# Kernel optimization log

Hardware: AMD Instinct MI355X
Metric: run time of the kernel (lower is better)

## Reference

```python
import jax, jax.numpy as jnp
import numpy as np


def _hfreq_mask(c, scale):
    # zeros over the centered (shifted) low-frequency band, ones elsewhere
    m = np.ones((c,), dtype=np.complex64)
    m[c // 2 - c // scale: c // 2 + c // scale] = 0
    return jnp.asarray(m).reshape(1, 1, 1, c)


def setup_inputs() -> dict:
    key = jax.random.key(0)
    x = jax.random.normal(key, (32, 38, 38, 728), dtype=jnp.float32)
    return {"x": x, "scale": 4}


def reference(x, scale):
    c = x.shape[-1]
    norm = jnp.asarray(np.sqrt(c), dtype=jnp.complex64)
    X = jnp.fft.fft(x.astype(jnp.complex64), axis=-1) / norm
    X = jnp.fft.fftshift(X, axes=-1)
    X = X * _hfreq_mask(c, scale)
    X = jnp.fft.ifftshift(X, axes=-1)
    y = jnp.fft.ifft(X, axis=-1) * norm
    y = jnp.real(y).astype(jnp.float32)
    return jax.nn.relu(y)
```

## Files before the change

### kernel.cpp

```cpp
#include <hip/hip_runtime.h>
#include <hip/hip_bf16.h>

#define CC 728
#define PP 364
#define KP 384
#define M_ROWS 46208
#define KT 12
#define NWG 2166

typedef __attribute__((ext_vector_type(8))) short bf16x8;
typedef __attribute__((ext_vector_type(8))) unsigned short ushort8;
typedef __attribute__((ext_vector_type(4))) float f32x4;

__device__ __forceinline__ unsigned short f2bf(float f) {
    unsigned int u = __float_as_uint(f);
    unsigned int r = u + 0x7fffu + ((u >> 16) & 1u);
    return (unsigned short)(r >> 16);
}

__device__ __forceinline__ void gload_lds16(const void* g, void* l) {
    __builtin_amdgcn_global_load_lds(
        (const __attribute__((address_space(1))) void*)g,
        (__attribute__((address_space(3))) void*)l,
        16, 0, 0);
}

__global__ void build_bt(unsigned short* __restrict__ bt1,
                         unsigned short* __restrict__ bt2) {
    int idx = blockIdx.x * blockDim.x + threadIdx.x;
    if (idx >= 2 * KP * KP) return;
    int mat = idx / (KP * KP);
    int rem = idx % (KP * KP);
    int n = rem / KP, k = rem % KP;
    float v = 0.f;
    if (n < PP && k < PP) {
        int m = n - k - (mat == 0 ? 1 : 0);
        if (m < 0) m += PP;
        int d = 2 * m + 1;
        float t = (float)(3.14159265358979323846 * (double)d / (double)CC);
        float s = ((d >> 1) & 1) ? 1.f : -1.f;
        v = s * cosf(t) / ((float)CC * sinf(t));
    }
    (mat == 0 ? bt1 : bt2)[n * KP + k] = f2bf(v);
}

__global__ __launch_bounds__(256) void gemm_relu(
        const float* __restrict__ x,
        const unsigned short* __restrict__ bt1,
        const unsigned short* __restrict__ bt2,
        float* __restrict__ out) {
    __shared__ unsigned short ldsE[64 * 32];
    __shared__ unsigned short ldsO[64 * 32];
    __shared__ unsigned short ldsB1[128 * 32];
    __shared__ unsigned short ldsB2[128 * 32];

    const int tid  = threadIdx.x;
    const int lane = tid & 63;
    const int wid  = tid >> 6;
    const int wr   = wid >> 1, wc = wid & 1;
    const int l15  = lane & 15, lhi = lane >> 4;

    const int NX = 8;
    int orig = blockIdx.x;
    int q = NWG / NX, r = NWG % NX;
    int xcd = orig % NX, local = orig / NX;
    int wgid = (xcd < r ? xcd * (q + 1) : r * (q + 1) + (xcd - r) * q) + local;
    const int bm  = (wgid / 3) * 64;
    const int bnp = (wgid % 3) * 128;

    f32x4 acc_e[2][4], acc_o[2][4];
#pragma unroll
    for (int i = 0; i < 2; ++i)
#pragma unroll
        for (int j = 0; j < 4; ++j)
#pragma unroll
            for (int rr = 0; rr < 4; ++rr) { acc_e[i][j][rr] = 0.f; acc_o[i][j][rr] = 0.f; }

    const int brow = tid >> 2;
    const int bc   = tid & 3;
    const int arow = tid >> 2;
    const int acx  = tid & 3;

    for (int kt = 0; kt < KT; ++kt) {
        const int k0 = kt * 32;

#pragma unroll
        for (int i = 0; i < 2; ++i) {
            int rr   = i * 64 + brow;
            int gsrc = (bc - (rr >> 1)) & 3;
            size_t so = (size_t)(bnp + rr) * KP + k0 + gsrc * 8;
            gload_lds16(bt1 + so, &ldsB1[(i * 256 + tid) * 8]);
            gload_lds16(bt2 + so, &ldsB2[(i * 256 + tid) * 8]);
        }

        float4 va[4];
        {
            int cb0 = 2 * k0 + acx * 16;
            const float* src = x + (size_t)(bm + arow) * CC + cb0;
#pragma unroll
            for (int i = 0; i < 4; ++i)
                va[i] = (cb0 + 4 * i < CC) ? ((const float4*)src)[i]
                                           : make_float4(0.f, 0.f, 0.f, 0.f);
        }

        {
            ushort8 oe, oo;
#pragma unroll
            for (int p = 0; p < 4; ++p) {
                float4 f = va[p];
                oe[2 * p]     = f2bf(f.x); oo[2 * p]     = f2bf(f.y);
                oe[2 * p + 1] = f2bf(f.z); oo[2 * p + 1] = f2bf(f.w);
            }
            int sc = (acx + (arow >> 1)) & 3;
            *(ushort8*)&ldsE[arow * 32 + sc * 8] = oe;
            *(ushort8*)&ldsO[arow * 32 + sc * 8] = oo;
        }
        __syncthreads();

        bf16x8 aE[2], aO[2], b1[4], b2[4];
#pragma unroll
        for (int mi = 0; mi < 2; ++mi) {
            int row = wr * 32 + mi * 16 + l15;
            int c   = (lhi + (row >> 1)) & 3;
            aE[mi] = *(const bf16x8*)&ldsE[row * 32 + c * 8];
            aO[mi] = *(const bf16x8*)&ldsO[row * 32 + c * 8];
        }
#pragma unroll
        for (int nj = 0; nj < 4; ++nj) {
            int row = wc * 64 + nj * 16 + l15;
            int c   = (lhi + (row >> 1)) & 3;
            b1[nj] = *(const bf16x8*)&ldsB1[row * 32 + c * 8];
            b2[nj] = *(const bf16x8*)&ldsB2[row * 32 + c * 8];
        }
#pragma unroll
        for (int mi = 0; mi < 2; ++mi)
#pragma unroll
            for (int nj = 0; nj < 4; ++nj) {
                acc_e[mi][nj] = __builtin_amdgcn_mfma_f32_16x16x32_bf16(
                    aO[mi], b1[nj], acc_e[mi][nj], 0, 0, 0);
                acc_o[mi][nj] = __builtin_amdgcn_mfma_f32_16x16x32_bf16(
                    aE[mi], b2[nj], acc_o[mi][nj], 0, 0, 0);
            }
        __syncthreads();
    }

#pragma unroll
    for (int mi = 0; mi < 2; ++mi) {
#pragma unroll
        for (int nj = 0; nj < 4; ++nj) {
            int colp = bnp + wc * 64 + nj * 16 + l15;
            if (colp < PP) {
#pragma unroll
                for (int rr = 0; rr < 4; ++rr) {
                    int rowg = bm + wr * 32 + mi * 16 + lhi * 4 + rr;
                    size_t base = (size_t)rowg * CC + 2 * colp;
                    float2 xv = *(const float2*)&x[base];
                    float2 o;
                    float ye = 0.5f * xv.x + acc_e[mi][nj][rr];
                    float yo = 0.5f * xv.y + acc_o[mi][nj][rr];
                    o.x = ye > 0.f ? ye : 0.f;
                    o.y = yo > 0.f ? yo : 0.f;
                    *(float2*)&out[base] = o;
                }
            }
        }
    }
}

extern "C" void kernel_launch(void* const* d_in, const int* in_sizes, int n_in,
                              void* d_out, int out_size, void* d_ws, size_t ws_size,
                              hipStream_t stream) {
    const float* x = (const float*)d_in[0];
    float* out = (float*)d_out;

    unsigned short* bt1 = (unsigned short*)d_ws;
    unsigned short* bt2 = bt1 + KP * KP;

    build_bt<<<(2 * KP * KP + 255) / 256, 256, 0, stream>>>(bt1, bt2);
    gemm_relu<<<NWG, 256, 0, stream>>>(x, bt1, bt2, out);
}
```

Measured before the change: 108.9 us.

## Drop LDS staging and load MFMA fragments straight from global memory

```diff
diff --git a/kernel.cpp b/kernel.cpp
--- a/kernel.cpp
+++ b/kernel.cpp
@@ -9,20 +9,12 @@
 #define NWG 2166
 
 typedef __attribute__((ext_vector_type(8))) short bf16x8;
-typedef __attribute__((ext_vector_type(8))) unsigned short ushort8;
 typedef __attribute__((ext_vector_type(4))) float f32x4;
 
 __device__ __forceinline__ unsigned short f2bf(float f) {
     unsigned int u = __float_as_uint(f);
     unsigned int r = u + 0x7fffu + ((u >> 16) & 1u);
     return (unsigned short)(r >> 16);
-}
-
-__device__ __forceinline__ void gload_lds16(const void* g, void* l) {
-    __builtin_amdgcn_global_load_lds(
-        (const __attribute__((address_space(1))) void*)g,
-        (__attribute__((address_space(3))) void*)l,
-        16, 0, 0);
 }
 
 __global__ void build_bt(unsigned short* __restrict__ bt1,
@@ -49,11 +41,6 @@
         const unsigned short* __restrict__ bt1,
         const unsigned short* __restrict__ bt2,
         float* __restrict__ out) {
-    __shared__ unsigned short ldsE[64 * 32];
-    __shared__ unsigned short ldsO[64 * 32];
-    __shared__ unsigned short ldsB1[128 * 32];
-    __shared__ unsigned short ldsB2[128 * 32];
-
     const int tid  = threadIdx.x;
     const int lane = tid & 63;
     const int wid  = tid >> 6;
@@ -65,99 +52,83 @@
     int q = NWG / NX, r = NWG % NX;
     int xcd = orig % NX, local = orig / NX;
     int wgid = (xcd < r ? xcd * (q + 1) : r * (q + 1) + (xcd - r) * q) + local;
-    const int bm  = (wgid / 3) * 64;
-    const int bnp = (wgid % 3) * 128;
+    const int bm  = (wgid / 6) * 128;
+    const int bnp = (wgid % 6) * 64;
 
-    f32x4 acc_e[2][4], acc_o[2][4];
+    f32x4 acc_e[4][2], acc_o[4][2];
 #pragma unroll
-    for (int i = 0; i < 2; ++i)
+    for (int i = 0; i < 4; ++i)
 #pragma unroll
-        for (int j = 0; j < 4; ++j)
+        for (int j = 0; j < 2; ++j)
 #pragma unroll
             for (int rr = 0; rr < 4; ++rr) { acc_e[i][j][rr] = 0.f; acc_o[i][j][rr] = 0.f; }
 
-    const int brow = tid >> 2;
-    const int bc   = tid & 3;
-    const int arow = tid >> 2;
-    const int acx  = tid & 3;
-
-    for (int kt = 0; kt < KT; ++kt) {
-        const int k0 = kt * 32;
-
+    const float* xrow[4];
 #pragma unroll
-        for (int i = 0; i < 2; ++i) {
-            int rr   = i * 64 + brow;
-            int gsrc = (bc - (rr >> 1)) & 3;
-            size_t so = (size_t)(bnp + rr) * KP + k0 + gsrc * 8;
-            gload_lds16(bt1 + so, &ldsB1[(i * 256 + tid) * 8]);
-            gload_lds16(bt2 + so, &ldsB2[(i * 256 + tid) * 8]);
-        }
-
-        float4 va[4];
-        {
-            int cb0 = 2 * k0 + acx * 16;
-            const float* src = x + (size_t)(bm + arow) * CC + cb0;
+    for (int mi = 0; mi < 4; ++mi)
+        xrow[mi] = x + (size_t)(bm + wr * 64 + mi * 16 + l15) * CC;
+    const unsigned short* btrow1[2];
+    const unsigned short* btrow2[2];
 #pragma unroll
-            for (int i = 0; i < 4; ++i)
-                va[i] = (cb0 + 4 * i < CC) ? ((const float4*)src)[i]
-                                           : make_float4(0.f, 0.f, 0.f, 0.f);
-        }
-
-        {
-            ushort8 oe, oo;
-#pragma unroll
-            for (int p = 0; p < 4; ++p) {
-                float4 f = va[p];
-                oe[2 * p]     = f2bf(f.x); oo[2 * p]     = f2bf(f.y);
-                oe[2 * p + 1] = f2bf(f.z); oo[2 * p + 1] = f2bf(f.w);
-            }
-            int sc = (acx + (arow >> 1)) & 3;
-            *(ushort8*)&ldsE[arow * 32 + sc * 8] = oe;
-            *(ushort8*)&ldsO[arow * 32 + sc * 8] = oo;
-        }
-        __syncthreads();
-
-        bf16x8 aE[2], aO[2], b1[4], b2[4];
-#pragma unroll
-        for (int mi = 0; mi < 2; ++mi) {
-            int row = wr * 32 + mi * 16 + l15;
-            int c   = (lhi + (row >> 1)) & 3;
-            aE[mi] = *(const bf16x8*)&ldsE[row * 32 + c * 8];
-            aO[mi] = *(const bf16x8*)&ldsO[row * 32 + c * 8];
-        }
-#pragma unroll
-        for (int nj = 0; nj < 4; ++nj) {
-            int row = wc * 64 + nj * 16 + l15;
-            int c   = (lhi + (row >> 1)) & 3;
-            b1[nj] = *(const bf16x8*)&ldsB1[row * 32 + c * 8];
-            b2[nj] = *(const bf16x8*)&ldsB2[row * 32 + c * 8];
-        }
-#pragma unroll
-        for (int mi = 0; mi < 2; ++mi)
-#pragma unroll
-            for (int nj = 0; nj < 4; ++nj) {
-                acc_e[mi][nj] = __builtin_amdgcn_mfma_f32_16x16x32_bf16(
-                    aO[mi], b1[nj], acc_e[mi][nj], 0, 0, 0);
-                acc_o[mi][nj] = __builtin_amdgcn_mfma_f32_16x16x32_bf16(
-                    aE[mi], b2[nj], acc_o[mi][nj], 0, 0, 0);
-            }
-        __syncthreads();
+    for (int nf = 0; nf < 2; ++nf) {
+        int n = bnp + wc * 32 + nf * 16 + l15;
+        btrow1[nf] = bt1 + (size_t)n * KP;
+        btrow2[nf] = bt2 + (size_t)n * KP;
     }
 
 #pragma unroll
-    for (int mi = 0; mi < 2; ++mi) {
+    for (int kt = 0; kt < KT; ++kt) {
+        const int pk0 = kt * 32 + lhi * 8;
+        const int cb0 = kt * 64 + lhi * 16;
+
+        bf16x8 b1f[2], b2f[2];
 #pragma unroll
-        for (int nj = 0; nj < 4; ++nj) {
-            int colp = bnp + wc * 64 + nj * 16 + l15;
+        for (int nf = 0; nf < 2; ++nf) {
+            b1f[nf] = *(const bf16x8*)(btrow1[nf] + pk0);
+            b2f[nf] = *(const bf16x8*)(btrow2[nf] + pk0);
+        }
+
+#pragma unroll
+        for (int mi = 0; mi < 4; ++mi) {
+            float4 f[4];
+#pragma unroll
+            for (int j = 0; j < 4; ++j) {
+                int cb = cb0 + j * 4;
+                f[j] = (cb < CC) ? ((const float4*)(xrow[mi] + cb0))[j]
+                                 : make_float4(0.f, 0.f, 0.f, 0.f);
+            }
+            union { bf16x8 v; unsigned int u[4]; } aE, aO;
+#pragma unroll
+            for (int j = 0; j < 4; ++j) {
+                asm("v_cvt_pk_bf16_f32 %0, %1, %2"
+                    : "=v"(aE.u[j]) : "v"(f[j].x), "v"(f[j].z));
+                asm("v_cvt_pk_bf16_f32 %0, %1, %2"
+                    : "=v"(aO.u[j]) : "v"(f[j].y), "v"(f[j].w));
+            }
+#pragma unroll
+            for (int nf = 0; nf < 2; ++nf) {
+                acc_e[mi][nf] = __builtin_amdgcn_mfma_f32_16x16x32_bf16(
+                    aO.v, b1f[nf], acc_e[mi][nf], 0, 0, 0);
+                acc_o[mi][nf] = __builtin_amdgcn_mfma_f32_16x16x32_bf16(
+                    aE.v, b2f[nf], acc_o[mi][nf], 0, 0, 0);
+            }
+        }
+    }
+
+#pragma unroll
+    for (int mi = 0; mi < 4; ++mi) {
+#pragma unroll
+        for (int nf = 0; nf < 2; ++nf) {
+            int colp = bnp + wc * 32 + nf * 16 + l15;
             if (colp < PP) {
 #pragma unroll
                 for (int rr = 0; rr < 4; ++rr) {
-                    int rowg = bm + wr * 32 + mi * 16 + lhi * 4 + rr;
+                    int rowg = bm + wr * 64 + mi * 16 + lhi * 4 + rr;
                     size_t base = (size_t)rowg * CC + 2 * colp;
                     float2 xv = *(const float2*)&x[base];
                     float2 o;
-                    float ye = 0.5f * xv.x + acc_e[mi][nj][rr];
-                    float yo = 0.5f * xv.y + acc_o[mi][nj][rr];
+                    float ye = 0.5f * xv.x + acc_e[mi][nf][rr];
+                    float yo = 0.5f * xv.y + acc_o[mi][nf][rr];
                     o.x = ye > 0.f ? ye : 0.f;
                     o.y = yo > 0.f ? yo : 0.f;
                     *(float2*)&out[base] = o;
```

After: 186.1 us. 1.71x slower.
